# Optimization experiments

Measured on AMD Instinct MI355X. Metric: run time of the kernel, lower is better.

The kernel has to match this reference:

```python
import jax, jax.numpy as jnp
import numpy as np

H = 1024      # hidden_size
V = 32000     # output_size (vocab)
BOS = 1


def setup_inputs() -> dict:
    key = jax.random.key(0)
    ks = jax.random.split(key, 12)
    B, S, T = 16, 128, 128
    s = 1.0 / np.sqrt(H)
    return {
        "encoder_outputs": jax.random.normal(ks[0], (B, S, H), jnp.float32),
        "encoder_hidden": jax.random.normal(ks[1], (1, B, H), jnp.float32),
        "tgt_tensor": jax.random.randint(ks[2], (B, T), 0, V),
        # embedding table
        "emb": jax.random.normal(ks[3], (V, H), jnp.float32) * 0.02,
        # additive attention (d2l style: Linear(..., bias=False))
        "Wq": jax.random.uniform(ks[4], (H, H), jnp.float32, -s, s),
        "Wk": jax.random.uniform(ks[5], (H, H), jnp.float32, -s, s),
        "v_att": jax.random.uniform(ks[6], (H,), jnp.float32, -s, s),
        # GRU (input size 2H): PyTorch layout W_ih [3H, 2H] (r,z,n), W_hh [3H, H]
        "W_ih": jax.random.uniform(ks[7], (3 * H, 2 * H), jnp.float32, -s, s),
        "W_hh": jax.random.uniform(ks[8], (3 * H, H), jnp.float32, -s, s),
        "b_ih": jax.random.uniform(ks[9], (3 * H,), jnp.float32, -s, s),
        "b_hh": jax.random.uniform(ks[10], (3 * H,), jnp.float32, -s, s),
        # output linear
        "W_out": jax.random.uniform(ks[11], (V, H), jnp.float32, -s, s),
        "b_out": jnp.zeros((V,), jnp.float32),
    }


def _decode(encoder_outputs, encoder_hidden, tgt_tensor,
            emb, Wq, Wk, v_att, W_ih, W_hh, b_ih, b_hh, W_out, b_out):
    B, S, _ = encoder_outputs.shape
    # decoder inputs under teacher forcing: [BOS, tgt[:, :-1]]  -> [B, T]
    dec_in = jnp.concatenate(
        [jnp.full((B, 1), BOS, dtype=tgt_tensor.dtype), tgt_tensor[:, :-1]], axis=1)
    # precompute key projection once: [B, S, H]
    kproj = jnp.einsum('bsh,gh->bsg', encoder_outputs, Wk)

    def step(h, x_t):  # h: [B,H], x_t: [B]
        e = emb[x_t]                                   # [B, H]
        q = h @ Wq.T                                   # [B, H]
        feat = jnp.tanh(q[:, None, :] + kproj)         # [B, S, H]
        scores = jnp.einsum('bsh,h->bs', feat, v_att)  # [B, S]
        w = jax.nn.softmax(scores, axis=-1)            # [B, S]
        ctx = jnp.einsum('bs,bsh->bh', w, encoder_outputs)  # [B, H]
        x = jnp.concatenate([e, ctx], axis=-1)         # [B, 2H]
        gx = x @ W_ih.T + b_ih                         # [B, 3H]
        gh = h @ W_hh.T + b_hh                         # [B, 3H]
        gx_r, gx_z, gx_n = jnp.split(gx, 3, axis=-1)
        gh_r, gh_z, gh_n = jnp.split(gh, 3, axis=-1)
        r = jax.nn.sigmoid(gx_r + gh_r)
        z = jax.nn.sigmoid(gx_z + gh_z)
        n = jnp.tanh(gx_n + r * gh_n)
        h_new = (1.0 - z) * n + z * h                  # [B, H]
        logits = h_new @ W_out.T + b_out               # [B, V]
        return h_new, (logits, w)

    h0 = encoder_hidden[0]                             # [B, H]
    hT, (logits, attw) = jax.lax.scan(step, h0, dec_in.T)  # time-major scan
    logits = jnp.transpose(logits, (1, 0, 2))          # [B, T, V]
    attw = jnp.transpose(attw, (1, 0, 2))              # [B, T, S]
    log_probs = jax.nn.log_softmax(logits, axis=-1)
    return log_probs, hT[None], attw


def reference(encoder_outputs, encoder_hidden, tgt_tensor,
              emb, Wq, Wk, v_att, W_ih, W_hh, b_ih, b_hh, W_out, b_out):
    return _decode(encoder_outputs, encoder_hidden, tgt_tensor,
                   emb, Wq, Wk, v_att, W_ih, W_hh, b_ih, b_hh, W_out, b_out)
```

## Files before the change

kernel.cpp:

```cpp
#include <hip/hip_runtime.h>

typedef unsigned short u16;
using f32x4  = __attribute__((ext_vector_type(4))) float;
using bf16x8 = __attribute__((ext_vector_type(8))) __bf16;

__device__ __forceinline__ float bf2f(u16 s){ return __builtin_bit_cast(float, (unsigned)s << 16); }
__device__ __forceinline__ float bflo(unsigned u){ return __builtin_bit_cast(float, u << 16); }
__device__ __forceinline__ float bfhi(unsigned u){ return __builtin_bit_cast(float, u & 0xffff0000u); }
__device__ __forceinline__ u16 f2bf(float f){
  unsigned u = __builtin_bit_cast(unsigned, f);
  unsigned r = u + 0x7fffu + ((u >> 16) & 1u);
  return (u16)(r >> 16);
}
__device__ __forceinline__ unsigned pk2(float x, float y){
  unsigned ux = __builtin_bit_cast(unsigned, x) + 0x8000u;
  unsigned uy = __builtin_bit_cast(unsigned, y) + 0x8000u;
  return (ux >> 16) | (uy & 0xffff0000u);
}
__device__ __forceinline__ float tanh_f(float x){ float e = __expf(2.f*x); return 1.f - 2.f/(e + 1.f); }
__device__ __forceinline__ float sigm(float x){ return 1.f/(1.f + __expf(-x)); }
__device__ __forceinline__ f32x4 mfma16(bf16x8 a, bf16x8 b, f32x4 c){
  return __builtin_amdgcn_mfma_f32_16x16x32_bf16(a, b, c, 0, 0, 0);
}
__device__ __forceinline__ bf16x8 ldg8(const u16* p){
  return __builtin_bit_cast(bf16x8, *(const uint4*)p);
}
__device__ __forceinline__ bf16x8 cvt8(const float* p){
  float4 a = *(const float4*)p, b = *(const float4*)(p + 4);
  uint4 r; r.x = pk2(a.x, a.y); r.y = pk2(a.z, a.w); r.z = pk2(b.x, b.y); r.w = pk2(b.z, b.w);
  return __builtin_bit_cast(bf16x8, r);
}
__device__ __forceinline__ void gld(const void* g, void* l){
  __builtin_amdgcn_global_load_lds(
      (const __attribute__((address_space(1))) void*)g,
      (__attribute__((address_space(3))) void*)l, 16, 0, 0);
}

__device__ __forceinline__ float coh_ld(const float* p){
  return __hip_atomic_load(p, __ATOMIC_RELAXED, __HIP_MEMORY_SCOPE_AGENT);
}
__device__ __forceinline__ void coh_st(float* p, float v){
  __hip_atomic_store(p, v, __ATOMIC_RELAXED, __HIP_MEMORY_SCOPE_AGENT);
}

template<int EPI, bool AF32, bool BF32>
__global__ __launch_bounds__(256) void gemm_bt(
    const void* __restrict__ Av, int lda,
    const void* __restrict__ Bv, int ldb,
    void* __restrict__ Cv, const float* __restrict__ bias,
    int K, int N)
{
  constexpr int ABYTES = AF32 ? 16384 : 8192;
  constexpr int BBYTES = BF32 ? 16384 : 8192;
  __shared__ __align__(16) unsigned char lsA[ABYTES];
  __shared__ __align__(16) unsigned char lsB[BBYTES];
  const int tid = threadIdx.x;
  const int wv = tid >> 6, l = tid & 63;
  const int m0 = blockIdx.y * 128, n0 = blockIdx.x * 128;
  const int wm = wv & 1, wn = wv >> 1;
  const f32x4 vzero = {0.f, 0.f, 0.f, 0.f};
  f32x4 acc[4][4];
#pragma unroll
  for (int i = 0; i < 4; ++i)
#pragma unroll
    for (int j = 0; j < 4; ++j) acc[i][j] = vzero;

  const float* gAf[4]; const u16* gAh[2]; void* dA[4];
  const float* gBf[4]; const u16* gBh[2]; void* dB[4];
  if constexpr (AF32){
    const float* A = (const float*)Av;
#pragma unroll
    for (int i = 0; i < 4; ++i){
      int e = (wv*4 + i)*64 + l;
      int kc = e >> 8, r = (e >> 1) & 127, h4 = (e & 1)*4;
      gAf[i] = A + (size_t)(m0 + r)*lda + kc*8 + h4;
      dA[i] = lsA + (wv*4 + i)*1024;
    }
  } else {
    const u16* A = (const u16*)Av;
#pragma unroll
    for (int i = 0; i < 2; ++i){
      int e = (wv*2 + i)*64 + l;
      int kc = e >> 7, r = e & 127;
      gAh[i] = A + (size_t)(m0 + r)*lda + kc*8;
      dA[i] = lsA + (wv*2 + i)*1024;
    }
  }
  if constexpr (BF32){
    const float* B = (const float*)Bv;
#pragma unroll
    for (int i = 0; i < 4; ++i){
      int e = (wv*4 + i)*64 + l;
      int kc = e >> 8, r = (e >> 1) & 127, h4 = (e & 1)*4;
      gBf[i] = B + (size_t)(n0 + r)*ldb + kc*8 + h4;
      dB[i] = lsB + (wv*4 + i)*1024;
    }
  } else {
    const u16* B = (const u16*)Bv;
#pragma unroll
    for (int i = 0; i < 2; ++i){
      int e = (wv*2 + i)*64 + l;
      int kc = e >> 7, r = e & 127;
      gBh[i] = B + (size_t)(n0 + r)*ldb + kc*8;
      dB[i] = lsB + (wv*2 + i)*1024;
    }
  }
  const int kq = l >> 4, li = l & 15;

  for (int k0 = 0; k0 < K; k0 += 32){
    __syncthreads();
    if constexpr (AF32){
#pragma unroll
      for (int i = 0; i < 4; ++i) gld(gAf[i] + k0, dA[i]);
    } else {
#pragma unroll
      for (int i = 0; i < 2; ++i) gld(gAh[i] + k0, dA[i]);
    }
    if constexpr (BF32){
#pragma unroll
      for (int i = 0; i < 4; ++i) gld(gBf[i] + k0, dB[i]);
    } else {
#pragma unroll
      for (int i = 0; i < 2; ++i) gld(gBh[i] + k0, dB[i]);
    }
    __syncthreads();
    bf16x8 aF[4], bF[4];
#pragma unroll
    for (int mi = 0; mi < 4; ++mi){
      int idx = kq*128 + wm*64 + mi*16 + li;
      if constexpr (AF32) aF[mi] = cvt8((const float*)lsA + idx*8);
      else                aF[mi] = ldg8((const u16*)lsA + idx*8);
    }
#pragma unroll
    for (int ni = 0; ni < 4; ++ni){
      int idx = kq*128 + wn*64 + ni*16 + li;
      if constexpr (BF32) bF[ni] = cvt8((const float*)lsB + idx*8);
      else                bF[ni] = ldg8((const u16*)lsB + idx*8);
    }
#pragma unroll
    for (int mi = 0; mi < 4; ++mi)
#pragma unroll
      for (int ni = 0; ni < 4; ++ni)
        acc[mi][ni] = mfma16(aF[mi], bF[ni], acc[mi][ni]);
  }

#pragma unroll
  for (int mi = 0; mi < 4; ++mi){
    const int mloc = wm*64 + mi*16 + kq*4;
#pragma unroll
    for (int ni = 0; ni < 4; ++ni){
      const int col = n0 + wn*64 + ni*16 + li;
      f32x4 v = acc[mi][ni];
      if constexpr (EPI == 1){
        float bb = bias ? bias[col] : 0.f;
        u16* C = (u16*)Cv;
#pragma unroll
        for (int r = 0; r < 4; ++r)
          C[(size_t)(m0 + mloc + r)*N + col] = f2bf(v[r] + bb);
      } else if constexpr (EPI == 2){
        float bb = bias[col];
        float* C = (float*)Cv;
#pragma unroll
        for (int r = 0; r < 4; ++r){
          int m = m0 + mloc + r;
          int orow = (m & 15)*128 + (m >> 4);
          C[(size_t)orow*N + col] = v[r] + bb;
        }
      } else {
        u16* C = (u16*)Cv;
        int m = m0 + mloc;
        int b = m >> 7, s = m & 127;
        unsigned w0 = (unsigned)f2bf(v[0]) | ((unsigned)f2bf(v[1]) << 16);
        unsigned w1 = (unsigned)f2bf(v[2]) | ((unsigned)f2bf(v[3]) << 16);
        uint2 pk; pk.x = w0; pk.y = w1;
        *(uint2*)(C + ((size_t)b*N + col)*128 + s) = pk;
      }
    }
  }
}

__global__ void cast_bf(const float* __restrict__ src, u16* __restrict__ dst, int n8){
  int i = blockIdx.x*256 + threadIdx.x;
  if (i < n8){
    float4 a = ((const float4*)src)[i*2], b = ((const float4*)src)[i*2 + 1];
    uint4 r; r.x = pk2(a.x, a.y); r.y = pk2(a.z, a.w); r.z = pk2(b.x, b.y); r.w = pk2(b.z, b.w);
    ((uint4*)dst)[i] = r;
  }
}

__global__ void gather_e(const int* __restrict__ tgt, const float* __restrict__ emb, u16* __restrict__ eall){
  int p = blockIdx.x;
  int t = p >> 4, b = p & 15;
  int tok = (t == 0) ? 1 : tgt[b*128 + (t - 1)];
  const float4* src = (const float4*)(emb + (size_t)tok*1024) + threadIdx.x*2;
  float4 a = src[0], c = src[1];
  uint4 r; r.x = pk2(a.x, a.y); r.y = pk2(a.z, a.w); r.z = pk2(c.x, c.y); r.w = pk2(c.z, c.w);
  ((uint4*)(eall + (size_t)p*1024))[threadIdx.x] = r;
}

__global__ void init_h(const float* __restrict__ eh, float* __restrict__ hf, int* __restrict__ bar){
  int i = blockIdx.x*256 + threadIdx.x;
  if (i < 1024) bar[i] = 0;
  hf[i] = eh[i];
}

struct RP {
  const u16 *Wc, *kproj, *Pt, *ge;
  const float *bhh, *vatt;
  float *q, *gh, *scores, *hf;
  u16 *hseq;
  float *outT, *attw;
  int *bar;
};

__device__ __forceinline__ void gbar(int* cnt, int target){
  __syncthreads();
  if (threadIdx.x == 0){
    __hip_atomic_fetch_add(cnt, 1, __ATOMIC_RELAXED, __HIP_MEMORY_SCOPE_AGENT);
    while (__hip_atomic_load(cnt, __ATOMIC_RELAXED, __HIP_MEMORY_SCOPE_AGENT) < target)
      __builtin_amdgcn_s_sleep(1);
  }
  __syncthreads();
}

__global__ __launch_bounds__(256) void rec_kernel(RP p){
  __shared__ float shm[1024];
  const int tid = threadIdx.x;
  const int blk = blockIdx.x;
  const int b = blk >> 4, ic = blk & 15;
  const int wv = tid >> 6, l = tid & 63;
  int* cnt = p.bar + b*32;
  int target = 0;

  const int r = ic*256 + tid;
  const u16* wr = p.Wc + (size_t)r*1024;
  float* qout = (r < 1024) ? (p.q + b*1024 + r) : (p.gh + b*3072 + (r - 1024));
  const float badd = (r < 1024) ? 0.f : p.bhh[r - 1024];

  float hreg = (tid < 64) ? p.hf[b*1024 + ic*64 + tid] : 0.f;

  for (int t = 0; t < 128; ++t){
    {
      const float* hfb = p.hf + b*1024 + tid*4;
      float4 hv;
      hv.x = coh_ld(hfb + 0); hv.y = coh_ld(hfb + 1);
      hv.z = coh_ld(hfb + 2); hv.w = coh_ld(hfb + 3);
      ((float4*)shm)[tid] = hv;
    }
    __syncthreads();
    {
      float a0 = 0.f, a1 = 0.f, a2 = 0.f, a3 = 0.f;
#pragma unroll 8
      for (int k0 = 0; k0 < 1024; k0 += 8){
        uint4 u = *(const uint4*)(wr + k0);
        a0 += shm[k0+0]*bflo(u.x) + shm[k0+1]*bfhi(u.x);
        a1 += shm[k0+2]*bflo(u.y) + shm[k0+3]*bfhi(u.y);
        a2 += shm[k0+4]*bflo(u.z) + shm[k0+5]*bfhi(u.z);
        a3 += shm[k0+6]*bflo(u.w) + shm[k0+7]*bfhi(u.w);
      }
      coh_st(qout, (a0 + a1) + (a2 + a3) + badd);
    }
    target += 16; gbar(cnt, target);

    {
      float qv[16];
      const float* qb = p.q + b*1024 + l*16;
#pragma unroll
      for (int j = 0; j < 16; ++j) qv[j] = coh_ld(qb + j);
      const float4* vp = (const float4*)(p.vatt) + l*4;
      float4 v0 = vp[0], v1 = vp[1], v2 = vp[2], v3 = vp[3];
#pragma unroll
      for (int si = 0; si < 2; ++si){
        int s = ic*8 + wv*2 + si;
        const uint4* kp = (const uint4*)(p.kproj + ((size_t)(b*128 + s))*1024) + l*2;
        uint4 ka = kp[0], kb = kp[1];
        float acc = 0.f;
        acc += v0.x*tanh_f(qv[0]  + bflo(ka.x)) + v0.y*tanh_f(qv[1]  + bfhi(ka.x));
        acc += v0.z*tanh_f(qv[2]  + bflo(ka.y)) + v0.w*tanh_f(qv[3]  + bfhi(ka.y));
        acc += v1.x*tanh_f(qv[4]  + bflo(ka.z)) + v1.y*tanh_f(qv[5]  + bfhi(ka.z));
        acc += v1.z*tanh_f(qv[6]  + bflo(ka.w)) + v1.w*tanh_f(qv[7]  + bfhi(ka.w));
        acc += v2.x*tanh_f(qv[8]  + bflo(kb.x)) + v2.y*tanh_f(qv[9]  + bfhi(kb.x));
        acc += v2.z*tanh_f(qv[10] + bflo(kb.y)) + v2.w*tanh_f(qv[11] + bfhi(kb.y));
        acc += v3.x*tanh_f(qv[12] + bflo(kb.z)) + v3.y*tanh_f(qv[13] + bfhi(kb.z));
        acc += v3.z*tanh_f(qv[14] + bflo(kb.w)) + v3.w*tanh_f(qv[15] + bfhi(kb.w));
#pragma unroll
        for (int o = 32; o; o >>= 1) acc += __shfl_xor(acc, o);
        if (l == 0) coh_st(p.scores + b*128 + s, acc);
      }
    }
    target += 16; gbar(cnt, target);

    {
      float* wf  = shm;
      float* gcv = shm + 128;
      if (wv == 0){
        float x0 = coh_ld(p.scores + b*128 + l);
        float x1 = coh_ld(p.scores + b*128 + 64 + l);
        float m = fmaxf(x0, x1);
#pragma unroll
        for (int o = 32; o; o >>= 1) m = fmaxf(m, __shfl_xor(m, o));
        float e0 = __expf(x0 - m), e1 = __expf(x1 - m);
        float sm = e0 + e1;
#pragma unroll
        for (int o = 32; o; o >>= 1) sm += __shfl_xor(sm, o);
        float inv = 1.f / sm;
        wf[l] = e0*inv; wf[64 + l] = e1*inv;
      }
      __syncthreads();
      if (tid < 192){
        int gate = tid >> 6, ii = tid & 63;
        int j = gate*1024 + ic*64 + ii;
        const uint4* pr = (const uint4*)(p.Pt + ((size_t)(b*3072 + j))*128);
        float acc = 0.f;
#pragma unroll
        for (int c = 0; c < 16; ++c){
          uint4 u = pr[c];
          const float* w8 = &wf[c*8];
          acc += w8[0]*bflo(u.x) + w8[1]*bfhi(u.x)
               + w8[2]*bflo(u.y) + w8[3]*bfhi(u.y)
               + w8[4]*bflo(u.z) + w8[5]*bfhi(u.z)
               + w8[6]*bflo(u.w) + w8[7]*bfhi(u.w);
        }
        gcv[tid] = acc;
      }
      __syncthreads();
      if (tid < 64){
        int i = ic*64 + tid;
        size_t mrow = (size_t)(t*16 + b);
        const u16* gep = p.ge + mrow*3072;
        float ger = bf2f(gep[i]), gez = bf2f(gep[i + 1024]), gen = bf2f(gep[i + 2048]);
        const float* ghp = p.gh + b*3072;
        float ghr = coh_ld(ghp + i);
        float ghz = coh_ld(ghp + i + 1024);
        float ghn = coh_ld(ghp + i + 2048);
        float rg = sigm(ger + gcv[tid] + ghr);
        float z  = sigm(gez + gcv[64 + tid] + ghz);
        float n  = tanh_f(gen + gcv[128 + tid] + rg*ghn);
        float hn = (1.f - z)*n + z*hreg;
        hreg = hn;
        coh_st(p.hf + b*1024 + i, hn);
        p.hseq[mrow*1024 + i] = f2bf(hn);
        if (t == 127) p.outT[b*1024 + i] = hn;
      }
      if (ic == 0 && tid < 128){
        p.attw[((size_t)(b*128 + t))*128 + tid] = wf[tid];
      }
    }
    target += 16; gbar(cnt, target);
  }
}

__global__ __launch_bounds__(256) void lse_kernel(const float* __restrict__ outp, float* __restrict__ lse){
  __shared__ float rm[256], rs[256];
  int r = blockIdx.x, tid = threadIdx.x;
  const float4* rp = (const float4*)(outp + (size_t)r*32000);
  float m = -3.0e38f, s = 0.f;
  for (int v = tid; v < 8000; v += 256){
    float4 x = rp[v];
    float mx = fmaxf(fmaxf(x.x, x.y), fmaxf(x.z, x.w));
    if (mx > m){ s *= __expf(m - mx); m = mx; }
    s += __expf(x.x - m) + __expf(x.y - m) + __expf(x.z - m) + __expf(x.w - m);
  }
  rm[tid] = m; rs[tid] = s;
  __syncthreads();
  for (int o = 128; o; o >>= 1){
    if (tid < o){
      float m2 = rm[tid + o], s2 = rs[tid + o], m1 = rm[tid], s1 = rs[tid];
      float M = fmaxf(m1, m2);
      rs[tid] = s1*__expf(m1 - M) + s2*__expf(m2 - M);
      rm[tid] = M;
    }
    __syncthreads();
  }
  if (tid == 0) lse[r] = rm[0] + __logf(rs[0]);
}

__global__ __launch_bounds__(256) void fixup_kernel(float* __restrict__ outp, const float* __restrict__ lse){
  int idx = blockIdx.x*256 + threadIdx.x;
  int r = idx / 8000;
  float L = lse[r];
  float4* p4 = (float4*)outp;
  float4 u = p4[idx];
  u.x -= L; u.y -= L; u.z -= L; u.w -= L;
  p4[idx] = u;
}

extern "C" void kernel_launch(void* const* d_in, const int* in_sizes, int n_in,
                              void* d_out, int out_size, void* d_ws, size_t ws_size,
                              hipStream_t stream) {
  (void)in_sizes; (void)n_in; (void)out_size; (void)ws_size;
  const float* eo   = (const float*)d_in[0];
  const float* eh   = (const float*)d_in[1];
  const int*   tgt  = (const int*)d_in[2];
  const float* emb  = (const float*)d_in[3];
  const float* Wq   = (const float*)d_in[4];
  const float* Wk   = (const float*)d_in[5];
  const float* vatt = (const float*)d_in[6];
  const float* Wih  = (const float*)d_in[7];
  const float* Whh  = (const float*)d_in[8];
  const float* bih  = (const float*)d_in[9];
  const float* bhh  = (const float*)d_in[10];
  const float* Wout = (const float*)d_in[11];
  const float* bout = (const float*)d_in[12];
  float* out = (float*)d_out;

  char* ws = (char*)d_ws;
  u16*  kproj = (u16*) (ws + 0);
  u16*  ge    = (u16*) (ws + 4194304);
  u16*  Pt    = (u16*) (ws + 16777216);
  u16*  eall  = (u16*) (ws + 29360128);
  u16*  hseq  = (u16*) (ws + 33554432);
  u16*  wqb   = (u16*) (ws + 37748736);
  u16*  whhb  = (u16*) (ws + 39845888);
  float* hf   = (float*)(ws + 46137344);
  int*  bar   = (int*)  (ws + 46202880);
  float* q    = (float*)(ws + 46235648);
  float* gh   = (float*)(ws + 46301184);
  float* sc   = (float*)(ws + 46497792);
  float* lse  = (float*)(ws + 46505984);

  float* outT = out + 65536000;
  float* attw = out + 65552384;

  cast_bf<<<512, 256, 0, stream>>>(Wq, wqb, 131072);
  cast_bf<<<1536, 256, 0, stream>>>(Whh, whhb, 393216);
  gather_e<<<2048, 128, 0, stream>>>(tgt, emb, eall);
  init_h<<<64, 256, 0, stream>>>(eh, hf, bar);

  gemm_bt<1, true, true><<<dim3(8, 16), 256, 0, stream>>>(eo, 1024, Wk, 1024, kproj, nullptr, 1024, 1024);
  gemm_bt<1, false, true><<<dim3(24, 16), 256, 0, stream>>>(eall, 1024, Wih, 2048, ge, bih, 1024, 3072);
  gemm_bt<3, true, true><<<dim3(24, 16), 256, 0, stream>>>(eo, 1024, Wih + 1024, 2048, Pt, nullptr, 1024, 3072);

  RP rp;
  rp.Wc = wqb; rp.kproj = kproj; rp.Pt = Pt; rp.ge = ge;
  rp.bhh = bhh; rp.vatt = vatt;
  rp.q = q; rp.gh = gh; rp.scores = sc; rp.hf = hf;
  rp.hseq = hseq; rp.outT = outT; rp.attw = attw;
  rp.bar = bar;
  void* kargs[] = { (void*)&rp };
  hipLaunchCooperativeKernel((void*)rec_kernel, dim3(256), dim3(256), kargs, 0, stream);

  gemm_bt<2, false, true><<<dim3(250, 16), 256, 0, stream>>>(hseq, 1024, Wout, 1024, out, bout, 1024, 32000);
  lse_kernel<<<2048, 256, 0, stream>>>(out, lse);
  fixup_kernel<<<64000, 256, 0, stream>>>(out, lse);
}
```

Measured before the change: 4.272 ms.

## Reorder weights so each block owns its hidden slice, removing one grid barrier per step

Wq and W_hh rows are now interleaved into one bf16 matrix, so each block computes the q slice and the three gate slices for the same 64 hidden indices and keeps them in shared memory. Each block then computes partial attention scores over its own 64-dim slice of q for all 128 positions and writes them to global memory. After a single barrier, every block sums the 16 partials and runs the softmax. This drops one of the three grid-wide barriers per timestep, along with the global round trips for q and gh. In exchange, every block redundantly reduces the partial scores and computes the softmax, and there is a new partial-score buffer.

```diff
diff --git a/kernel.cpp b/kernel.cpp
--- a/kernel.cpp
+++ b/kernel.cpp
@@ -179,13 +179,16 @@
   }
 }
 
-__global__ void cast_bf(const float* __restrict__ src, u16* __restrict__ dst, int n8){
-  int i = blockIdx.x*256 + threadIdx.x;
-  if (i < n8){
-    float4 a = ((const float4*)src)[i*2], b = ((const float4*)src)[i*2 + 1];
-    uint4 r; r.x = pk2(a.x, a.y); r.y = pk2(a.z, a.w); r.z = pk2(b.x, b.y); r.w = pk2(b.z, b.w);
-    ((uint4*)dst)[i] = r;
-  }
+__global__ void cast_w2(const float* __restrict__ Wq, const float* __restrict__ Whh, u16* __restrict__ Wc2){
+  int r2 = blockIdx.x;
+  int ic = r2 >> 8, lr = r2 & 255;
+  const float* src;
+  if (lr < 64) src = Wq + (size_t)(ic*64 + lr)*1024;
+  else { int gate = (lr - 64) >> 6, i = (lr - 64) & 63; src = Whh + (size_t)(gate*1024 + ic*64 + i)*1024; }
+  const float4* s4 = (const float4*)src + threadIdx.x*2;
+  float4 a = s4[0], c = s4[1];
+  uint4 r; r.x = pk2(a.x, a.y); r.y = pk2(a.z, a.w); r.z = pk2(c.x, c.y); r.w = pk2(c.z, c.w);
+  ((uint4*)(Wc2 + (size_t)r2*1024))[threadIdx.x] = r;
 }
 
 __global__ void gather_e(const int* __restrict__ tgt, const float* __restrict__ emb, u16* __restrict__ eall){
@@ -205,9 +208,9 @@
 }
 
 struct RP {
-  const u16 *Wc, *kproj, *Pt, *ge;
+  const u16 *Wc2, *kproj, *Pt, *ge;
   const float *bhh, *vatt;
-  float *q, *gh, *scores, *hf;
+  float *psc, *hf;
   u16 *hseq;
   float *outT, *attw;
   int *bar;
@@ -224,7 +227,13 @@
 }
 
 __global__ __launch_bounds__(256) void rec_kernel(RP p){
-  __shared__ float shm[1024];
+  __shared__ float hshm[1024];
+  __shared__ float qv[64];
+  __shared__ float ghv[192];
+  __shared__ float vv[64];
+  __shared__ float sraw[128];
+  __shared__ float wf[128];
+  __shared__ float gcv[192];
   const int tid = threadIdx.x;
   const int blk = blockIdx.x;
   const int b = blk >> 4, ic = blk & 15;
@@ -232,10 +241,17 @@
   int* cnt = p.bar + b*32;
   int target = 0;
 
-  const int r = ic*256 + tid;
-  const u16* wr = p.Wc + (size_t)r*1024;
-  float* qout = (r < 1024) ? (p.q + b*1024 + r) : (p.gh + b*3072 + (r - 1024));
-  const float badd = (r < 1024) ? 0.f : p.bhh[r - 1024];
+  const u16* wr = p.Wc2 + ((size_t)(ic*256 + tid))*1024;
+  float badd = 0.f;
+  if (tid >= 64){
+    int gate = (tid - 64) >> 6, i = (tid - 64) & 63;
+    badd = p.bhh[gate*1024 + ic*64 + i];
+  }
+  if (tid < 64) vv[tid] = p.vatt[ic*64 + tid];
+
+  const int s_pair = tid >> 1, half = tid & 1;
+  const u16* kbase = p.kproj + ((size_t)(b*128 + s_pair))*1024 + ic*64 + half*32;
+  float* pscw = p.psc + (b*16 + ic)*128 + s_pair;
 
   float hreg = (tid < 64) ? p.hf[b*1024 + ic*64 + tid] : 0.f;
 
@@ -245,7 +261,7 @@
       float4 hv;
       hv.x = coh_ld(hfb + 0); hv.y = coh_ld(hfb + 1);
       hv.z = coh_ld(hfb + 2); hv.w = coh_ld(hfb + 3);
-      ((float4*)shm)[tid] = hv;
+      ((float4*)hshm)[tid] = hv;
     }
     __syncthreads();
     {
@@ -253,98 +269,86 @@
 #pragma unroll 8
       for (int k0 = 0; k0 < 1024; k0 += 8){
         uint4 u = *(const uint4*)(wr + k0);
-        a0 += shm[k0+0]*bflo(u.x) + shm[k0+1]*bfhi(u.x);
-        a1 += shm[k0+2]*bflo(u.y) + shm[k0+3]*bfhi(u.y);
-        a2 += shm[k0+4]*bflo(u.z) + shm[k0+5]*bfhi(u.z);
-        a3 += shm[k0+6]*bflo(u.w) + shm[k0+7]*bfhi(u.w);
+        a0 += hshm[k0+0]*bflo(u.x) + hshm[k0+1]*bfhi(u.x);
+        a1 += hshm[k0+2]*bflo(u.y) + hshm[k0+3]*bfhi(u.y);
+        a2 += hshm[k0+4]*bflo(u.z) + hshm[k0+5]*bfhi(u.z);
+        a3 += hshm[k0+6]*bflo(u.w) + hshm[k0+7]*bfhi(u.w);
       }
-      coh_st(qout, (a0 + a1) + (a2 + a3) + badd);
+      float r = (a0 + a1) + (a2 + a3) + badd;
+      if (tid < 64) qv[tid] = r; else ghv[tid - 64] = r;
+    }
+    __syncthreads();
+    {
+      float acc = 0.f;
+#pragma unroll
+      for (int c = 0; c < 4; ++c){
+        uint4 u = *(const uint4*)(kbase + c*8);
+        int j = half*32 + c*8;
+        acc += vv[j+0]*tanh_f(qv[j+0] + bflo(u.x)) + vv[j+1]*tanh_f(qv[j+1] + bfhi(u.x));
+        acc += vv[j+2]*tanh_f(qv[j+2] + bflo(u.y)) + vv[j+3]*tanh_f(qv[j+3] + bfhi(u.y));
+        acc += vv[j+4]*tanh_f(qv[j+4] + bflo(u.z)) + vv[j+5]*tanh_f(qv[j+5] + bfhi(u.z));
+        acc += vv[j+6]*tanh_f(qv[j+6] + bflo(u.w)) + vv[j+7]*tanh_f(qv[j+7] + bfhi(u.w));
+      }
+      acc += __shfl_xor(acc, 1);
+      if (half == 0) coh_st(pscw, acc);
     }
     target += 16; gbar(cnt, target);
 
-    {
-      float qv[16];
-      const float* qb = p.q + b*1024 + l*16;
-#pragma unroll
-      for (int j = 0; j < 16; ++j) qv[j] = coh_ld(qb + j);
-      const float4* vp = (const float4*)(p.vatt) + l*4;
-      float4 v0 = vp[0], v1 = vp[1], v2 = vp[2], v3 = vp[3];
-#pragma unroll
-      for (int si = 0; si < 2; ++si){
-        int s = ic*8 + wv*2 + si;
-        const uint4* kp = (const uint4*)(p.kproj + ((size_t)(b*128 + s))*1024) + l*2;
-        uint4 ka = kp[0], kb = kp[1];
-        float acc = 0.f;
-        acc += v0.x*tanh_f(qv[0]  + bflo(ka.x)) + v0.y*tanh_f(qv[1]  + bfhi(ka.x));
-        acc += v0.z*tanh_f(qv[2]  + bflo(ka.y)) + v0.w*tanh_f(qv[3]  + bfhi(ka.y));
-        acc += v1.x*tanh_f(qv[4]  + bflo(ka.z)) + v1.y*tanh_f(qv[5]  + bfhi(ka.z));
-        acc += v1.z*tanh_f(qv[6]  + bflo(ka.w)) + v1.w*tanh_f(qv[7]  + bfhi(ka.w));
-        acc += v2.x*tanh_f(qv[8]  + bflo(kb.x)) + v2.y*tanh_f(qv[9]  + bfhi(kb.x));
-        acc += v2.z*tanh_f(qv[10] + bflo(kb.y)) + v2.w*tanh_f(qv[11] + bfhi(kb.y));
-        acc += v3.x*tanh_f(qv[12] + bflo(kb.z)) + v3.y*tanh_f(qv[13] + bfhi(kb.z));
-        acc += v3.z*tanh_f(qv[14] + bflo(kb.w)) + v3.w*tanh_f(qv[15] + bfhi(kb.w));
-#pragma unroll
-        for (int o = 32; o; o >>= 1) acc += __shfl_xor(acc, o);
-        if (l == 0) coh_st(p.scores + b*128 + s, acc);
+    if (tid < 128){
+      const float* pr = p.psc + b*2048 + tid;
+      float s0 = 0.f;
+#pragma unroll
+      for (int j = 0; j < 16; ++j) s0 += coh_ld(pr + j*128);
+      sraw[tid] = s0;
+    }
+    __syncthreads();
+    if (wv == 0){
+      float x0 = sraw[l], x1 = sraw[64 + l];
+      float m = fmaxf(x0, x1);
+#pragma unroll
+      for (int o = 32; o; o >>= 1) m = fmaxf(m, __shfl_xor(m, o));
+      float e0 = __expf(x0 - m), e1 = __expf(x1 - m);
+      float sm = e0 + e1;
+#pragma unroll
+      for (int o = 32; o; o >>= 1) sm += __shfl_xor(sm, o);
+      float inv = 1.f / sm;
+      wf[l] = e0*inv; wf[64 + l] = e1*inv;
+    }
+    __syncthreads();
+    if (tid < 192){
+      int gate = tid >> 6, ii = tid & 63;
+      int j = gate*1024 + ic*64 + ii;
+      const uint4* pr = (const uint4*)(p.Pt + ((size_t)(b*3072 + j))*128);
+      float acc = 0.f;
+#pragma unroll
+      for (int c = 0; c < 16; ++c){
+        uint4 u = pr[c];
+        const float* w8 = &wf[c*8];
+        acc += w8[0]*bflo(u.x) + w8[1]*bfhi(u.x)
+             + w8[2]*bflo(u.y) + w8[3]*bfhi(u.y)
+             + w8[4]*bflo(u.z) + w8[5]*bfhi(u.z)
+             + w8[6]*bflo(u.w) + w8[7]*bfhi(u.w);
       }
-    }
-    target += 16; gbar(cnt, target);
-
-    {
-      float* wf  = shm;
-      float* gcv = shm + 128;
-      if (wv == 0){
-        float x0 = coh_ld(p.scores + b*128 + l);
-        float x1 = coh_ld(p.scores + b*128 + 64 + l);
-        float m = fmaxf(x0, x1);
-#pragma unroll
-        for (int o = 32; o; o >>= 1) m = fmaxf(m, __shfl_xor(m, o));
-        float e0 = __expf(x0 - m), e1 = __expf(x1 - m);
-        float sm = e0 + e1;
-#pragma unroll
-        for (int o = 32; o; o >>= 1) sm += __shfl_xor(sm, o);
-        float inv = 1.f / sm;
-        wf[l] = e0*inv; wf[64 + l] = e1*inv;
-      }
-      __syncthreads();
-      if (tid < 192){
-        int gate = tid >> 6, ii = tid & 63;
-        int j = gate*1024 + ic*64 + ii;
-        const uint4* pr = (const uint4*)(p.Pt + ((size_t)(b*3072 + j))*128);
-        float acc = 0.f;
-#pragma unroll
-        for (int c = 0; c < 16; ++c){
-          uint4 u = pr[c];
-          const float* w8 = &wf[c*8];
-          acc += w8[0]*bflo(u.x) + w8[1]*bfhi(u.x)
-               + w8[2]*bflo(u.y) + w8[3]*bfhi(u.y)
-               + w8[4]*bflo(u.z) + w8[5]*bfhi(u.z)
-               + w8[6]*bflo(u.w) + w8[7]*bfhi(u.w);
-        }
-        gcv[tid] = acc;
-      }
-      __syncthreads();
-      if (tid < 64){
-        int i = ic*64 + tid;
-        size_t mrow = (size_t)(t*16 + b);
-        const u16* gep = p.ge + mrow*3072;
-        float ger = bf2f(gep[i]), gez = bf2f(gep[i + 1024]), gen = bf2f(gep[i + 2048]);
-        const float* ghp = p.gh + b*3072;
-        float ghr = coh_ld(ghp + i);
-        float ghz = coh_ld(ghp + i + 1024);
-        float ghn = coh_ld(ghp + i + 2048);
-        float rg = sigm(ger + gcv[tid] + ghr);
-        float z  = sigm(gez + gcv[64 + tid] + ghz);
-        float n  = tanh_f(gen + gcv[128 + tid] + rg*ghn);
-        float hn = (1.f - z)*n + z*hreg;
-        hreg = hn;
-        coh_st(p.hf + b*1024 + i, hn);
-        p.hseq[mrow*1024 + i] = f2bf(hn);
-        if (t == 127) p.outT[b*1024 + i] = hn;
-      }
-      if (ic == 0 && tid < 128){
-        p.attw[((size_t)(b*128 + t))*128 + tid] = wf[tid];
-      }
+      gcv[tid] = acc;
+    }
+    __syncthreads();
+    if (tid < 64){
+      int i = ic*64 + tid;
+      size_t mrow = (size_t)(t*16 + b);
+      const u16* gep = p.ge + mrow*3072;
+      float ger = bf2f(gep[i]), gez = bf2f(gep[i + 1024]), gen = bf2f(gep[i + 2048]);
+      float ghr = ghv[tid], ghz = ghv[64 + tid], ghn = ghv[128 + tid];
+      float rg = sigm(ger + gcv[tid] + ghr);
+      float z  = sigm(gez + gcv[64 + tid] + ghz);
+      float n  = tanh_f(gen + gcv[128 + tid] + rg*ghn);
+      float hn = (1.f - z)*n + z*hreg;
+      hreg = hn;
+      coh_st(p.hf + b*1024 + i, hn);
+      p.hseq[mrow*1024 + i] = f2bf(hn);
+      if (t == 127) p.outT[b*1024 + i] = hn;
+    }
+    if (ic == 0 && tid < 128){
+      p.attw[((size_t)(b*128 + t))*128 + tid] = wf[tid];
     }
     target += 16; gbar(cnt, target);
   }
@@ -410,20 +414,16 @@
   u16*  Pt    = (u16*) (ws + 16777216);
   u16*  eall  = (u16*) (ws + 29360128);
   u16*  hseq  = (u16*) (ws + 33554432);
-  u16*  wqb   = (u16*) (ws + 37748736);
-  u16*  whhb  = (u16*) (ws + 39845888);
+  u16*  wc2   = (u16*) (ws + 37748736);
   float* hf   = (float*)(ws + 46137344);
   int*  bar   = (int*)  (ws + 46202880);
-  float* q    = (float*)(ws + 46235648);
-  float* gh   = (float*)(ws + 46301184);
-  float* sc   = (float*)(ws + 46497792);
+  float* psc  = (float*)(ws + 46235648);
   float* lse  = (float*)(ws + 46505984);
 
   float* outT = out + 65536000;
   float* attw = out + 65552384;
 
-  cast_bf<<<512, 256, 0, stream>>>(Wq, wqb, 131072);
-  cast_bf<<<1536, 256, 0, stream>>>(Whh, whhb, 393216);
+  cast_w2<<<4096, 128, 0, stream>>>(Wq, Whh, wc2);
   gather_e<<<2048, 128, 0, stream>>>(tgt, emb, eall);
   init_h<<<64, 256, 0, stream>>>(eh, hf, bar);
 
@@ -432,9 +432,9 @@
   gemm_bt<3, true, true><<<dim3(24, 16), 256, 0, stream>>>(eo, 1024, Wih + 1024, 2048, Pt, nullptr, 1024, 3072);
 
   RP rp;
-  rp.Wc = wqb; rp.kproj = kproj; rp.Pt = Pt; rp.ge = ge;
+  rp.Wc2 = wc2; rp.kproj = kproj; rp.Pt = Pt; rp.ge = ge;
   rp.bhh = bhh; rp.vatt = vatt;
-  rp.q = q; rp.gh = gh; rp.scores = sc; rp.hf = hf;
+  rp.psc = psc; rp.hf = hf;
   rp.hseq = hseq; rp.outT = outT; rp.attw = attw;
   rp.bar = bar;
   void* kargs[] = { (void*)&rp };
```

After: 4.004 ms. 1.07x faster.
